# Optimization experiments

Measured on AMD Instinct MI355X. Metric: run time of the kernel, lower is better.

Reference implementation:

```python
import jax, jax.numpy as jnp
import numpy as np

N, D, DIN, S, R = 128, 2560, 5120, 16, 160  # users, d_model, d_inner, d_state, dt_rank


def setup_inputs() -> dict:
    key = jax.random.key(0)
    ks = jax.random.split(key, 16)
    f = lambda k, shape, s: jax.random.normal(k, shape, dtype=jnp.float32) * s
    return {
        "x": f(ks[0], (1, 1, N, D), 1.0),
        "conv_state0": f(ks[1], (1, 1, N, DIN), 0.1),
        "conv_state1": f(ks[2], (1, 1, N, DIN), 0.1),
        "conv_state2": f(ks[3], (1, 1, N, DIN), 0.1),
        "conv_state3": f(ks[4], (1, 1, N, DIN), 0.1),
        "ssm_state": f(ks[5], (N, DIN, S), 0.1),
        "ssm_proj": f(ks[6], (D, DIN), 0.02),
        "mlp_proj": f(ks[7], (D, DIN), 0.02),
        "down_proj": f(ks[8], (DIN, D), 0.02),
        "conv_w": f(ks[9], (4, DIN), 0.2),
        "conv_bias": f(ks[10], (DIN,), 0.1),
        "x_proj_w": f(ks[11], (DIN, R + 2 * S), 0.02),
        "dt_proj_w": f(ks[12], (R, DIN), 0.05),
        "dt_proj_b": f(ks[13], (DIN,), 0.1),
        "A_log": jnp.log(jnp.broadcast_to(jnp.arange(1, S + 1, dtype=jnp.float32), (DIN, S))),
        "D_param": jnp.ones((DIN,), jnp.float32),
    }


def reference(x, conv_state0, conv_state1, conv_state2, conv_state3, ssm_state,
              ssm_proj, mlp_proj, down_proj, conv_w, conv_bias,
              x_proj_w, dt_proj_w, dt_proj_b, A_log, D_param):
    r = dt_proj_w.shape[0]
    s = A_log.shape[1]
    x2 = x[0, 0]                         # (N, D)
    xs = x2 @ ssm_proj                   # (N, DIN) in_proj (ssm half)
    # shifted conv state window: oldest state (conv_state0) is dropped
    states = (conv_state1[0, 0], conv_state2[0, 0], conv_state3[0, 0], xs)
    conv_out = conv_bias + conv_w[0] * states[0] + conv_w[1] * states[1] \
        + conv_w[2] * states[2] + conv_w[3] * states[3]   # (N, DIN)
    u = jax.nn.silu(conv_out)
    # selective-scan single step (TtMambaSSM)
    proj = u @ x_proj_w                  # (N, R + 2S)
    dt = jax.nn.softplus(proj[:, :r] @ dt_proj_w + dt_proj_b)  # (N, DIN)
    Bm = proj[:, r:r + s]                # (N, S)
    Cm = proj[:, r + s:]                 # (N, S)
    A = -jnp.exp(A_log)                  # (DIN, S)
    dA = jnp.exp(dt[:, :, None] * A[None])                     # (N, DIN, S)
    h = dA * ssm_state + dt[:, :, None] * Bm[:, None, :] * u[:, :, None]
    y = jnp.einsum('nds,ns->nd', h, Cm) + D_param * u          # (N, DIN)
    # residual/gate branch and output projection (note: no silu on res, as in source)
    res = x2 @ mlp_proj                  # (N, DIN)
    out = (y * res) @ down_proj          # (N, D)
    return out[None, None]               # (1, 1, N, D)
```

## Files before the change

kernel.cpp:

```cpp
#include <hip/hip_runtime.h>

using u16 = unsigned short;
using u32 = unsigned int;

typedef __attribute__((ext_vector_type(8))) short short8;
typedef __attribute__((ext_vector_type(4))) float floatx4;

constexpr int TOKENS = 128;
constexpr int DM = 2560;
constexpr int DI = 5120;
constexpr int NS = 16;
constexpr int NR = 160;
constexpr int NP = 192;

constexpr size_t XS_OFF   = 0;
constexpr size_t RES_OFF  = XS_OFF  + (size_t)TOKENS * DI;
constexpr size_t U_OFF    = RES_OFF + (size_t)TOKENS * DI;
constexpr size_t DT_OFF   = U_OFF   + (size_t)TOKENS * DI;
constexpr size_t PROJ_OFF = DT_OFF  + (size_t)TOKENS * DI;
constexpr size_t OACC_OFF = PROJ_OFF + (size_t)TOKENS * NP;

__device__ __forceinline__ float bf2f(u16 h) {
  u32 u = ((u32)h) << 16;
  return __builtin_bit_cast(float, u);
}
__device__ __forceinline__ u16 f2bf(float f) {
  u32 u = __builtin_bit_cast(u32, f);
  u += 0x7FFFu + ((u >> 16) & 1u);
  return (u16)(u >> 16);
}
__device__ __forceinline__ u32 pk2(float a, float b) {
  return (u32)f2bf(a) | ((u32)f2bf(b) << 16);
}
__device__ __forceinline__ float ldsc(const void* p, size_t i, bool bf) {
  return bf ? bf2f(((const u16*)p)[i]) : ((const float*)p)[i];
}
__device__ __forceinline__ uint4 ld8(const void* p, size_t i, bool bf) {
  if (bf) return *(const uint4*)((const u16*)p + i);
  const float4* f = (const float4*)((const float*)p + i);
  float4 a = f[0], b = f[1];
  return (uint4){pk2(a.x, a.y), pk2(a.z, a.w), pk2(b.x, b.y), pk2(b.z, b.w)};
}

struct GemmP {
  const void* A; int lda; int a_ws;
  const void* B; const void* B2;
  float* C; float* C2;
  int ldb; int ldc;
  int ksteps;
  int nx_half;
  const u32* probe;
};

__global__ __launch_bounds__(256, 4) void gemm_k(GemmP p) {
  __shared__ u16 As[128 * 40];
  __shared__ u16 Bs[32 * 64];

  const bool bf = (p.probe[0] != 0u);
  const int tid = threadIdx.x;
  const int bx = blockIdx.x;
  const void* B = p.B; float* C = p.C;
  int nblk = bx;
  if (bx >= p.nx_half) { B = p.B2; C = p.C2; nblk = bx - p.nx_half; }
  const int n0 = nblk * 64;
  const int kstart = blockIdx.y * p.ksteps * 32;

  const int wave = tid >> 6, lane = tid & 63;
  const int q = lane >> 4, l16 = lane & 15;
  const int wx = wave & 1, wy = wave >> 1;

  const bool a_f32 = p.a_ws || !bf;
  const int am = (tid + 0) >> 2, asg = tid & 3;
  const int am2 = (tid + 256) >> 2;
  const int bk = tid >> 3, bsg = tid & 7;

  floatx4 acc[4][2];
#pragma unroll
  for (int mi = 0; mi < 4; mi++)
#pragma unroll
    for (int ni = 0; ni < 2; ni++) acc[mi][ni] = (floatx4){0.f, 0.f, 0.f, 0.f};

  uint4 aW[2], bW;
  auto load_tiles = [&](int ks, uint4* aO, uint4& bO) {
    const int kbase = kstart + ks * 32;
    if (!a_f32) {
      aO[0] = *(const uint4*)((const u16*)p.A + (size_t)am * p.lda + kbase + asg * 8);
      aO[1] = *(const uint4*)((const u16*)p.A + (size_t)am2 * p.lda + kbase + asg * 8);
    } else {
      const float4* f0 = (const float4*)((const float*)p.A + (size_t)am * p.lda + kbase + asg * 8);
      const float4* f1 = (const float4*)((const float*)p.A + (size_t)am2 * p.lda + kbase + asg * 8);
      float4 a0 = f0[0], a1 = f0[1], b0 = f1[0], b1 = f1[1];
      aO[0] = (uint4){pk2(a0.x, a0.y), pk2(a0.z, a0.w), pk2(a1.x, a1.y), pk2(a1.z, a1.w)};
      aO[1] = (uint4){pk2(b0.x, b0.y), pk2(b0.z, b0.w), pk2(b1.x, b1.y), pk2(b1.z, b1.w)};
    }
    bO = ld8(B, (size_t)(kbase + bk) * p.ldb + n0 + bsg * 8, bf);
  };

  load_tiles(0, aW, bW);

  for (int ks = 0;;) {
    __syncthreads();
    *(uint4*)&As[am * 40 + asg * 8] = aW[0];
    *(uint4*)&As[am2 * 40 + asg * 8] = aW[1];
    {
      int off = ((bsg << 4) + ((bk >> 3) << 5)) & 127;
      *(uint4*)&Bs[bk * 64 + (off >> 1)] = bW;
    }
    __syncthreads();

    uint4 aN[2], bN;
    const bool more = (ks + 1 < p.ksteps);
    if (more) load_tiles(ks + 1, aN, bN);

    short8 afr[4];
#pragma unroll
    for (int mi = 0; mi < 4; mi++)
      afr[mi] = __builtin_bit_cast(short8,
          *(const uint4*)&As[(wy * 64 + mi * 16 + l16) * 40 + q * 8]);
    short8 bfr[2];
#pragma unroll
    for (int ni = 0; ni < 2; ni++) {
      int nl2 = (wx * 32 + ni * 16 + l16) * 2;
      int boff = (nl2 + (q << 5)) & 127;
      const u16* bp = &Bs[q * 512 + (boff >> 1)];
      short8 b;
#pragma unroll
      for (int j = 0; j < 8; j++) b[j] = (short)bp[j * 64];
      bfr[ni] = b;
    }
#pragma unroll
    for (int mi = 0; mi < 4; mi++)
#pragma unroll
      for (int ni = 0; ni < 2; ni++)
        acc[mi][ni] = __builtin_amdgcn_mfma_f32_16x16x32_bf16(
            afr[mi], bfr[ni], acc[mi][ni], 0, 0, 0);

    if (!more) break;
    aW[0] = aN[0]; aW[1] = aN[1]; bW = bN;
    ks++;
  }

#pragma unroll
  for (int ni = 0; ni < 2; ni++) {
    int col = n0 + wx * 32 + ni * 16 + l16;
#pragma unroll
    for (int mi = 0; mi < 4; mi++) {
      floatx4 v = acc[mi][ni];
#pragma unroll
      for (int r = 0; r < 4; r++) {
        int row = wy * 64 + mi * 16 + q * 4 + r;
        atomicAdd(&C[(size_t)row * p.ldc + col], v[r]);
      }
    }
  }
}

__global__ __launch_bounds__(256) void epi_u_k(
    const float* __restrict__ xs_acc, const void* __restrict__ cs1,
    const void* __restrict__ cs2, const void* __restrict__ cs3,
    const void* __restrict__ cw, const void* __restrict__ cb,
    float* __restrict__ u, const u32* __restrict__ probe) {
  const bool bf = (probe[0] != 0u);
  const int n = blockIdx.y;
  const int d = blockIdx.x * 256 + threadIdx.x;
  const size_t nd = (size_t)n * DI + d;
  float cv = ldsc(cb, d, bf) + ldsc(cw, d, bf) * ldsc(cs1, nd, bf) +
             ldsc(cw, DI + d, bf) * ldsc(cs2, nd, bf) +
             ldsc(cw, 2 * DI + d, bf) * ldsc(cs3, nd, bf) +
             ldsc(cw, 3 * DI + d, bf) * xs_acc[nd];
  u[nd] = cv / (1.0f + __expf(-cv));
}

__global__ __launch_bounds__(256) void ssm_k(
    const void* __restrict__ sstate, const void* __restrict__ alog,
    const void* __restrict__ dparam, const void* __restrict__ dtb,
    const float* __restrict__ proj, const float* __restrict__ dtacc,
    const float* __restrict__ u, const float* __restrict__ res,
    float* __restrict__ z, const u32* __restrict__ probe) {
  const bool bf = (probe[0] != 0u);
  const int n = blockIdx.y;
  const int d = blockIdx.x * 256 + threadIdx.x;
  __shared__ float Bsh[NS], Csh[NS];
  if (threadIdx.x < NS)
    Bsh[threadIdx.x] = proj[(size_t)n * NP + NR + threadIdx.x];
  else if (threadIdx.x < 2 * NS)
    Csh[threadIdx.x - NS] = proj[(size_t)n * NP + NR + threadIdx.x];
  __syncthreads();
  const size_t nd = (size_t)n * DI + d;
  const float uv = u[nd], rv = res[nd];
  float sv = dtacc[nd] + ldsc(dtb, d, bf);
  const float dtv = (sv > 20.0f) ? sv : log1pf(__expf(sv));

  float stf[16], alf[16];
  if (bf) {
    u16 st[16], al[16];
    const uint4* sp = (const uint4*)((const u16*)sstate + nd * 16);
    *(uint4*)&st[0] = sp[0]; *(uint4*)&st[8] = sp[1];
    const uint4* ap = (const uint4*)((const u16*)alog + (size_t)d * 16);
    *(uint4*)&al[0] = ap[0]; *(uint4*)&al[8] = ap[1];
#pragma unroll
    for (int s = 0; s < 16; s++) { stf[s] = bf2f(st[s]); alf[s] = bf2f(al[s]); }
  } else {
    const float4* sp = (const float4*)((const float*)sstate + nd * 16);
    const float4* ap = (const float4*)((const float*)alog + (size_t)d * 16);
#pragma unroll
    for (int i = 0; i < 4; i++) {
      float4 s4 = sp[i], a4 = ap[i];
      stf[i * 4 + 0] = s4.x; stf[i * 4 + 1] = s4.y; stf[i * 4 + 2] = s4.z; stf[i * 4 + 3] = s4.w;
      alf[i * 4 + 0] = a4.x; alf[i * 4 + 1] = a4.y; alf[i * 4 + 2] = a4.z; alf[i * 4 + 3] = a4.w;
    }
  }
  float y = 0.f;
#pragma unroll
  for (int s = 0; s < 16; s++) {
    float Aa = -__expf(alf[s]);
    float dA = __expf(dtv * Aa);
    float h = dA * stf[s] + dtv * Bsh[s] * uv;
    y += h * Csh[s];
  }
  y += ldsc(dparam, d, bf) * uv;
  z[nd] = y * rv;
}

__global__ __launch_bounds__(256) void cvt_k(const float* __restrict__ in,
                                             void* __restrict__ out, int n,
                                             const u32* __restrict__ probe) {
  const bool bf = (probe[0] != 0u);
  int i = blockIdx.x * 256 + threadIdx.x;
  if (i < n) {
    if (bf) ((u16*)out)[i] = f2bf(in[i]);
    else    ((float*)out)[i] = in[i];
  }
}

extern "C" void kernel_launch(void* const* d_in, const int* in_sizes, int n_in,
                              void* d_out, int out_size, void* d_ws, size_t ws_size,
                              hipStream_t stream) {
  const void* x         = d_in[0];
  const void* cs1       = d_in[2];
  const void* cs2       = d_in[3];
  const void* cs3       = d_in[4];
  const void* ssm_state = d_in[5];
  const void* ssm_proj  = d_in[6];
  const void* mlp_proj  = d_in[7];
  const void* down_proj = d_in[8];
  const void* conv_w    = d_in[9];
  const void* conv_b    = d_in[10];
  const void* x_proj_w  = d_in[11];
  const void* dt_proj_w = d_in[12];
  const void* dt_proj_b = d_in[13];
  const void* A_log     = d_in[14];
  const void* D_param   = d_in[15];
  const u32*  probe     = (const u32*)A_log;

  float* ws     = (float*)d_ws;
  float* xs_acc = ws + XS_OFF;
  float* z      = ws + XS_OFF;
  float* res    = ws + RES_OFF;
  float* u      = ws + U_OFF;
  float* dtacc  = ws + DT_OFF;
  float* proj   = ws + PROJ_OFF;
  float* oacc   = ws + OACC_OFF;

  hipMemsetAsync(xs_acc, 0, (size_t)TOKENS * DI * sizeof(float), stream);
  hipMemsetAsync(res,    0, (size_t)TOKENS * DI * sizeof(float), stream);
  hipMemsetAsync(dtacc,  0, (size_t)TOKENS * DI * sizeof(float), stream);
  hipMemsetAsync(proj,   0, (size_t)TOKENS * NP * sizeof(float), stream);
  hipMemsetAsync(oacc,   0, (size_t)TOKENS * DM * sizeof(float), stream);

  {
    GemmP p{};
    p.A = x; p.lda = DM; p.a_ws = 0;
    p.B = ssm_proj; p.B2 = mlp_proj;
    p.C = xs_acc; p.C2 = res;
    p.ldb = DI; p.ldc = DI;
    p.ksteps = DM / 32 / 8; p.nx_half = 80;
    p.probe = probe;
    gemm_k<<<dim3(160, 8), 256, 0, stream>>>(p);
  }
  epi_u_k<<<dim3(DI / 256, TOKENS), 256, 0, stream>>>(
      xs_acc, cs1, cs2, cs3, conv_w, conv_b, u, probe);
  {
    GemmP p{};
    p.A = u; p.lda = DI; p.a_ws = 1;
    p.B = x_proj_w; p.B2 = nullptr;
    p.C = proj; p.C2 = nullptr;
    p.ldb = NP; p.ldc = NP;
    p.ksteps = 4; p.nx_half = 1 << 30;
    p.probe = probe;
    gemm_k<<<dim3(3, 40), 256, 0, stream>>>(p);
  }
  {
    GemmP p{};
    p.A = proj; p.lda = NP; p.a_ws = 1;
    p.B = dt_proj_w; p.B2 = nullptr;
    p.C = dtacc; p.C2 = nullptr;
    p.ldb = DI; p.ldc = DI;
    p.ksteps = 1; p.nx_half = 1 << 30;
    p.probe = probe;
    gemm_k<<<dim3(DI / 64, 5), 256, 0, stream>>>(p);
  }
  ssm_k<<<dim3(DI / 256, TOKENS), 256, 0, stream>>>(
      ssm_state, A_log, D_param, dt_proj_b, proj, dtacc, u, res, z, probe);
  {
    GemmP p{};
    p.A = z; p.lda = DI; p.a_ws = 1;
    p.B = down_proj; p.B2 = nullptr;
    p.C = oacc; p.C2 = nullptr;
    p.ldb = DM; p.ldc = DM;
    p.ksteps = DI / 32 / 16; p.nx_half = 1 << 30;
    p.probe = probe;
    gemm_k<<<dim3(DM / 64, 16), 256, 0, stream>>>(p);
  }
  cvt_k<<<dim3((out_size + 255) / 256), 256, 0, stream>>>(oacc, d_out, out_size, probe);
}
```

Measured before the change: 322.2 us.

## Template GEMM on K-tile depth, swizzle LDS, cut split-K, vectorize elementwise kernels

The GEMM kernel becomes a template on the K-tile depth (64 or 32). Shared-memory layouts are XOR-swizzled so the B operand is stored transposed and read as one 16-byte vector instead of eight scalar LDS reads. Split-K factors are reduced (8→2, 40→20, 16→4), and the dt GEMM drops split-K entirely, writing results directly without atomics, which removes one memset. The elementwise conv/silu and output conversion kernels are vectorized to 8 elements per thread. Fewer split-K blocks cut atomic traffic but leave fewer blocks to fill the GPU.

```diff
diff --git a/kernel.cpp b/kernel.cpp
--- a/kernel.cpp
+++ b/kernel.cpp
@@ -40,6 +40,19 @@
   const float4* f = (const float4*)((const float*)p + i);
   float4 a = f[0], b = f[1];
   return (uint4){pk2(a.x, a.y), pk2(a.z, a.w), pk2(b.x, b.y), pk2(b.z, b.w)};
+}
+__device__ __forceinline__ void ld8f(const void* p, size_t i, bool bf, float* o) {
+  if (bf) {
+    uint4 v = *(const uint4*)((const u16*)p + i);
+    const u16* h = (const u16*)&v;
+#pragma unroll
+    for (int e = 0; e < 8; e++) o[e] = bf2f(h[e]);
+  } else {
+    const float4* f = (const float4*)((const float*)p + i);
+    float4 a = f[0], b = f[1];
+    o[0] = a.x; o[1] = a.y; o[2] = a.z; o[3] = a.w;
+    o[4] = b.x; o[5] = b.y; o[6] = b.z; o[7] = b.w;
+  }
 }
 
 struct GemmP {
@@ -49,12 +62,21 @@
   int ldb; int ldc;
   int ksteps;
   int nx_half;
+  int atomic;
   const u32* probe;
 };
 
-__global__ __launch_bounds__(256, 4) void gemm_k(GemmP p) {
-  __shared__ u16 As[128 * 40];
-  __shared__ u16 Bs[32 * 64];
+template <int BK>
+__global__ __launch_bounds__(256, 4) void gemm_t(GemmP p) {
+  constexpr int NBLK = BK / 8;
+  constexpr int MASK = NBLK - 1;
+  constexpr int KK = BK / 32;
+  constexpr int LOGN = (BK == 64) ? 3 : 2;
+  constexpr int RP = 256 / NBLK;
+  constexpr int PA = 128 / RP;
+
+  __shared__ __align__(16) u16 As[128 * BK];
+  __shared__ __align__(16) u16 Bs[64 * BK];
 
   const bool bf = (p.probe[0] != 0u);
   const int tid = threadIdx.x;
@@ -63,16 +85,19 @@
   int nblk = bx;
   if (bx >= p.nx_half) { B = p.B2; C = p.C2; nblk = bx - p.nx_half; }
   const int n0 = nblk * 64;
-  const int kstart = blockIdx.y * p.ksteps * 32;
+  const int kstart = blockIdx.y * p.ksteps * BK;
 
   const int wave = tid >> 6, lane = tid & 63;
   const int q = lane >> 4, l16 = lane & 15;
   const int wx = wave & 1, wy = wave >> 1;
 
   const bool a_f32 = p.a_ws || !bf;
-  const int am = (tid + 0) >> 2, asg = tid & 3;
-  const int am2 = (tid + 256) >> 2;
-  const int bk = tid >> 3, bsg = tid & 7;
+
+  const int ac = tid & MASK;
+  const int am0 = tid >> LOGN;
+  const int bc = tid & 7;
+  const int br = tid >> 3;
+  const int bn8 = bc * 8;
 
   floatx4 acc[4][2];
 #pragma unroll
@@ -80,76 +105,131 @@
 #pragma unroll
     for (int ni = 0; ni < 2; ni++) acc[mi][ni] = (floatx4){0.f, 0.f, 0.f, 0.f};
 
-  uint4 aW[2], bW;
-  auto load_tiles = [&](int ks, uint4* aO, uint4& bO) {
-    const int kbase = kstart + ks * 32;
-    if (!a_f32) {
-      aO[0] = *(const uint4*)((const u16*)p.A + (size_t)am * p.lda + kbase + asg * 8);
-      aO[1] = *(const uint4*)((const u16*)p.A + (size_t)am2 * p.lda + kbase + asg * 8);
+  uint4 aR[PA];
+  uint4 bR[KK];
+
+  auto load_tiles = [&](int ks) {
+    const int kb = kstart + ks * BK;
+#pragma unroll
+    for (int pa = 0; pa < PA; pa++) {
+      const int m = am0 + pa * RP;
+      const size_t off = (size_t)m * p.lda + kb + ac * 8;
+      if (!a_f32) {
+        aR[pa] = *(const uint4*)((const u16*)p.A + off);
+      } else {
+        const float4* f = (const float4*)((const float*)p.A + off);
+        float4 x0 = f[0], x1 = f[1];
+        aR[pa] = (uint4){pk2(x0.x, x0.y), pk2(x0.z, x0.w),
+                         pk2(x1.x, x1.y), pk2(x1.z, x1.w)};
+      }
+    }
+    if constexpr (BK == 64) {
+      bR[0] = ld8(B, (size_t)(kb + 2 * br) * p.ldb + n0 + bn8, bf);
+      bR[1] = ld8(B, (size_t)(kb + 2 * br + 1) * p.ldb + n0 + bn8, bf);
     } else {
-      const float4* f0 = (const float4*)((const float*)p.A + (size_t)am * p.lda + kbase + asg * 8);
-      const float4* f1 = (const float4*)((const float*)p.A + (size_t)am2 * p.lda + kbase + asg * 8);
-      float4 a0 = f0[0], a1 = f0[1], b0 = f1[0], b1 = f1[1];
-      aO[0] = (uint4){pk2(a0.x, a0.y), pk2(a0.z, a0.w), pk2(a1.x, a1.y), pk2(a1.z, a1.w)};
-      aO[1] = (uint4){pk2(b0.x, b0.y), pk2(b0.z, b0.w), pk2(b1.x, b1.y), pk2(b1.z, b1.w)};
-    }
-    bO = ld8(B, (size_t)(kbase + bk) * p.ldb + n0 + bsg * 8, bf);
+      bR[0] = ld8(B, (size_t)(kb + br) * p.ldb + n0 + bn8, bf);
+    }
   };
 
-  load_tiles(0, aW, bW);
+  auto store_tiles = [&]() {
+#pragma unroll
+    for (int pa = 0; pa < PA; pa++) {
+      const int m = am0 + pa * RP;
+      *(uint4*)&As[m * BK + ((ac ^ (m & MASK)) << 3)] = aR[pa];
+    }
+    if constexpr (BK == 64) {
+      const u16* lo = (const u16*)&bR[0];
+      const u16* hi = (const u16*)&bR[1];
+      const int k2 = 2 * br;
+#pragma unroll
+      for (int j = 0; j < 8; j++) {
+        const int n = bn8 + j;
+        const int blk = (k2 >> 3) ^ ((n ^ (n >> 3)) & MASK);
+        *(u32*)&Bs[n * BK + (blk << 3) + (k2 & 7)] =
+            (u32)lo[j] | ((u32)hi[j] << 16);
+      }
+    } else {
+      const u16* lo = (const u16*)&bR[0];
+#pragma unroll
+      for (int j = 0; j < 8; j++) {
+        const int n = bn8 + j;
+        const int blk = (br >> 3) ^ ((n ^ (n >> 3)) & MASK);
+        Bs[n * BK + (blk << 3) + (br & 7)] = lo[j];
+      }
+    }
+  };
+
+  const int swA = l16 & MASK;
+  const int arow = (wy * 64 + l16) * BK;
+  int nrow[2], swb[2];
+#pragma unroll
+  for (int ni = 0; ni < 2; ni++) {
+    const int n = wx * 32 + ni * 16 + l16;
+    nrow[ni] = n * BK;
+    swb[ni] = (n ^ (n >> 3)) & MASK;
+  }
+
+  load_tiles(0);
 
   for (int ks = 0;;) {
     __syncthreads();
-    *(uint4*)&As[am * 40 + asg * 8] = aW[0];
-    *(uint4*)&As[am2 * 40 + asg * 8] = aW[1];
-    {
-      int off = ((bsg << 4) + ((bk >> 3) << 5)) & 127;
-      *(uint4*)&Bs[bk * 64 + (off >> 1)] = bW;
-    }
+    store_tiles();
     __syncthreads();
-
-    uint4 aN[2], bN;
     const bool more = (ks + 1 < p.ksteps);
-    if (more) load_tiles(ks + 1, aN, bN);
-
-    short8 afr[4];
-#pragma unroll
-    for (int mi = 0; mi < 4; mi++)
-      afr[mi] = __builtin_bit_cast(short8,
-          *(const uint4*)&As[(wy * 64 + mi * 16 + l16) * 40 + q * 8]);
-    short8 bfr[2];
+    if (more) load_tiles(ks + 1);
+
+#pragma unroll
+    for (int kk = 0; kk < KK; kk++) {
+      const int kq = kk * 4 + q;
+      const int ao = (kq ^ swA) << 3;
+      short8 a[4];
+#pragma unroll
+      for (int mi = 0; mi < 4; mi++)
+        a[mi] = __builtin_bit_cast(short8,
+            *(const uint4*)&As[arow + mi * 16 * BK + ao]);
+      short8 b[2];
+#pragma unroll
+      for (int ni = 0; ni < 2; ni++)
+        b[ni] = __builtin_bit_cast(short8,
+            *(const uint4*)&Bs[nrow[ni] + ((kq ^ swb[ni]) << 3)]);
+#pragma unroll
+      for (int mi = 0; mi < 4; mi++)
+#pragma unroll
+        for (int ni = 0; ni < 2; ni++)
+          acc[mi][ni] = __builtin_amdgcn_mfma_f32_16x16x32_bf16(
+              a[mi], b[ni], acc[mi][ni], 0, 0, 0);
+    }
+
+    if (!more) break;
+    ks++;
+  }
+
+  if (p.atomic) {
 #pragma unroll
     for (int ni = 0; ni < 2; ni++) {
-      int nl2 = (wx * 32 + ni * 16 + l16) * 2;
-      int boff = (nl2 + (q << 5)) & 127;
-      const u16* bp = &Bs[q * 512 + (boff >> 1)];
-      short8 b;
-#pragma unroll
-      for (int j = 0; j < 8; j++) b[j] = (short)bp[j * 64];
-      bfr[ni] = b;
-    }
-#pragma unroll
-    for (int mi = 0; mi < 4; mi++)
-#pragma unroll
-      for (int ni = 0; ni < 2; ni++)
-        acc[mi][ni] = __builtin_amdgcn_mfma_f32_16x16x32_bf16(
-            afr[mi], bfr[ni], acc[mi][ni], 0, 0, 0);
-
-    if (!more) break;
-    aW[0] = aN[0]; aW[1] = aN[1]; bW = bN;
-    ks++;
-  }
-
-#pragma unroll
-  for (int ni = 0; ni < 2; ni++) {
-    int col = n0 + wx * 32 + ni * 16 + l16;
-#pragma unroll
-    for (int mi = 0; mi < 4; mi++) {
-      floatx4 v = acc[mi][ni];
-#pragma unroll
-      for (int r = 0; r < 4; r++) {
-        int row = wy * 64 + mi * 16 + q * 4 + r;
-        atomicAdd(&C[(size_t)row * p.ldc + col], v[r]);
+      const int col = n0 + wx * 32 + ni * 16 + l16;
+#pragma unroll
+      for (int mi = 0; mi < 4; mi++) {
+        floatx4 v = acc[mi][ni];
+#pragma unroll
+        for (int r = 0; r < 4; r++) {
+          const int row = wy * 64 + mi * 16 + q * 4 + r;
+          atomicAdd(&C[(size_t)row * p.ldc + col], v[r]);
+        }
+      }
+    }
+  } else {
+#pragma unroll
+    for (int ni = 0; ni < 2; ni++) {
+      const int col = n0 + wx * 32 + ni * 16 + l16;
+#pragma unroll
+      for (int mi = 0; mi < 4; mi++) {
+        floatx4 v = acc[mi][ni];
+#pragma unroll
+        for (int r = 0; r < 4; r++) {
+          const int row = wy * 64 + mi * 16 + q * 4 + r;
+          C[(size_t)row * p.ldc + col] = v[r];
+        }
       }
     }
   }
@@ -161,14 +241,36 @@
     const void* __restrict__ cw, const void* __restrict__ cb,
     float* __restrict__ u, const u32* __restrict__ probe) {
   const bool bf = (probe[0] != 0u);
-  const int n = blockIdx.y;
-  const int d = blockIdx.x * 256 + threadIdx.x;
-  const size_t nd = (size_t)n * DI + d;
-  float cv = ldsc(cb, d, bf) + ldsc(cw, d, bf) * ldsc(cs1, nd, bf) +
-             ldsc(cw, DI + d, bf) * ldsc(cs2, nd, bf) +
-             ldsc(cw, 2 * DI + d, bf) * ldsc(cs3, nd, bf) +
-             ldsc(cw, 3 * DI + d, bf) * xs_acc[nd];
-  u[nd] = cv / (1.0f + __expf(-cv));
+  const int idx = blockIdx.x * 256 + threadIdx.x;
+  const int n = idx / (DI / 8);
+  const int d0 = (idx - n * (DI / 8)) * 8;
+  const size_t nd = (size_t)n * DI + d0;
+  float xv[8];
+  {
+    const float4* f = (const float4*)(xs_acc + nd);
+    float4 a = f[0], b = f[1];
+    xv[0] = a.x; xv[1] = a.y; xv[2] = a.z; xv[3] = a.w;
+    xv[4] = b.x; xv[5] = b.y; xv[6] = b.z; xv[7] = b.w;
+  }
+  float c1[8], c2[8], c3[8], w0[8], w1[8], w2[8], w3[8], bb[8];
+  ld8f(cs1, nd, bf, c1);
+  ld8f(cs2, nd, bf, c2);
+  ld8f(cs3, nd, bf, c3);
+  ld8f(cw, (size_t)0 * DI + d0, bf, w0);
+  ld8f(cw, (size_t)1 * DI + d0, bf, w1);
+  ld8f(cw, (size_t)2 * DI + d0, bf, w2);
+  ld8f(cw, (size_t)3 * DI + d0, bf, w3);
+  ld8f(cb, d0, bf, bb);
+  float o[8];
+#pragma unroll
+  for (int e = 0; e < 8; e++) {
+    float cv = bb[e] + w0[e] * c1[e] + w1[e] * c2[e] + w2[e] * c3[e] +
+               w3[e] * xv[e];
+    o[e] = cv / (1.0f + __expf(-cv));
+  }
+  float4* uo = (float4*)(u + nd);
+  uo[0] = (float4){o[0], o[1], o[2], o[3]};
+  uo[1] = (float4){o[4], o[5], o[6], o[7]};
 }
 
 __global__ __launch_bounds__(256) void ssm_k(
@@ -226,10 +328,22 @@
                                              void* __restrict__ out, int n,
                                              const u32* __restrict__ probe) {
   const bool bf = (probe[0] != 0u);
-  int i = blockIdx.x * 256 + threadIdx.x;
-  if (i < n) {
-    if (bf) ((u16*)out)[i] = f2bf(in[i]);
-    else    ((float*)out)[i] = in[i];
+  const int i0 = (blockIdx.x * 256 + threadIdx.x) * 8;
+  if (i0 + 8 <= n) {
+    const float4* f = (const float4*)(in + i0);
+    float4 a = f[0], b = f[1];
+    if (bf) {
+      uint4 v = {pk2(a.x, a.y), pk2(a.z, a.w), pk2(b.x, b.y), pk2(b.z, b.w)};
+      *(uint4*)((u16*)out + i0) = v;
+    } else {
+      float4* o = (float4*)((float*)out + i0);
+      o[0] = a; o[1] = b;
+    }
+  } else {
+    for (int i = i0; i < n; i++) {
+      if (bf) ((u16*)out)[i] = f2bf(in[i]);
+      else    ((float*)out)[i] = in[i];
+    }
   }
 }
 
@@ -264,7 +378,6 @@
 
   hipMemsetAsync(xs_acc, 0, (size_t)TOKENS * DI * sizeof(float), stream);
   hipMemsetAsync(res,    0, (size_t)TOKENS * DI * sizeof(float), stream);
-  hipMemsetAsync(dtacc,  0, (size_t)TOKENS * DI * sizeof(float), stream);
   hipMemsetAsync(proj,   0, (size_t)TOKENS * NP * sizeof(float), stream);
   hipMemsetAsync(oacc,   0, (size_t)TOKENS * DM * sizeof(float), stream);
 
@@ -274,11 +387,11 @@
     p.B = ssm_proj; p.B2 = mlp_proj;
     p.C = xs_acc; p.C2 = res;
     p.ldb = DI; p.ldc = DI;
-    p.ksteps = DM / 32 / 8; p.nx_half = 80;
+    p.ksteps = 20; p.nx_half = 80; p.atomic = 1;
     p.probe = probe;
-    gemm_k<<<dim3(160, 8), 256, 0, stream>>>(p);
-  }
-  epi_u_k<<<dim3(DI / 256, TOKENS), 256, 0, stream>>>(
+    gemm_t<64><<<dim3(160, 2), 256, 0, stream>>>(p);
+  }
+  epi_u_k<<<dim3(TOKENS * DI / 8 / 256), 256, 0, stream>>>(
       xs_acc, cs1, cs2, cs3, conv_w, conv_b, u, probe);
   {
     GemmP p{};
@@ -286,9 +399,9 @@
     p.B = x_proj_w; p.B2 = nullptr;
     p.C = proj; p.C2 = nullptr;
     p.ldb = NP; p.ldc = NP;
-    p.ksteps = 4; p.nx_half = 1 << 30;
+    p.ksteps = 4; p.nx_half = 1 << 30; p.atomic = 1;
     p.probe = probe;
-    gemm_k<<<dim3(3, 40), 256, 0, stream>>>(p);
+    gemm_t<64><<<dim3(3, 20), 256, 0, stream>>>(p);
   }
   {
     GemmP p{};
@@ -296,9 +409,9 @@
     p.B = dt_proj_w; p.B2 = nullptr;
     p.C = dtacc; p.C2 = nullptr;
     p.ldb = DI; p.ldc = DI;
-    p.ksteps = 1; p.nx_half = 1 << 30;
+    p.ksteps = 5; p.nx_half = 1 << 30; p.atomic = 0;
     p.probe = probe;
-    gemm_k<<<dim3(DI / 64, 5), 256, 0, stream>>>(p);
+    gemm_t<32><<<dim3(DI / 64, 1), 256, 0, stream>>>(p);
   }
   ssm_k<<<dim3(DI / 256, TOKENS), 256, 0, stream>>>(
       ssm_state, A_log, D_param, dt_proj_b, proj, dtacc, u, res, z, probe);
@@ -308,9 +421,9 @@
     p.B = down_proj; p.B2 = nullptr;
     p.C = oacc; p.C2 = nullptr;
     p.ldb = DM; p.ldc = DM;
-    p.ksteps = DI / 32 / 16; p.nx_half = 1 << 30;
+    p.ksteps = 20; p.nx_half = 1 << 30; p.atomic = 1;
     p.probe = probe;
-    gemm_k<<<dim3(DM / 64, 16), 256, 0, stream>>>(p);
-  }
-  cvt_k<<<dim3((out_size + 255) / 256), 256, 0, stream>>>(oacc, d_out, out_size, probe);
-}
+    gemm_t<64><<<dim3(DM / 64, 4), 256, 0, stream>>>(p);
+  }
+  cvt_k<<<dim3((out_size / 8 + 255) / 256), 256, 0, stream>>>(oacc, d_out, out_size, probe);
+}
```

New measurement: 389.4 us. 20.9% more time.
